# Performance work log

Measured on AMD Instinct MI355X. Metric: run time of the kernel, lower is better.

## Reference

```python
import jax, jax.numpy as jnp
import numpy as np

EPS = 0.05        # idw eps from __init__
RMS_EPS = 1e-6    # rmsnorm eps
B, NTOT, N, GS, C = 128, 129, 128, 16, 384


def setup_inputs() -> dict:
    key = jax.random.key(0)
    k1, k2, k3, k4 = jax.random.split(key, 4)
    f = jax.random.normal(k1, (B, NTOT, C), dtype=jnp.float32)
    distance = jax.random.uniform(k2, (B, N, GS), dtype=jnp.float32)
    rf = jax.random.normal(k3, (NTOT, C), dtype=jnp.float32)
    knorm_w = jnp.ones((C,), dtype=jnp.float32)
    idx = jax.random.randint(k4, (B, N, GS), 0, B * N, dtype=jnp.int64)
    return {"f": f, "distance": distance, "rf": rf, "knorm_w": knorm_w, "idx": idx}


def _rmsnorm(x, w):
    rms = jnp.sqrt(jnp.mean(x * x, axis=-1, keepdims=True) + RMS_EPS)
    return x / rms * w


def reference(f, distance, rf, knorm_w, idx):
    t = f.shape[1] - N                       # number of cls tokens (1)
    cls_token = f[:, :t, :]                  # [B, t, C]
    x = f[:, t:, :]                          # [B, 128, C]
    rfx = rf[t:]                             # [128, C]
    c = rfx                                  # adabias: per-point bias broadcast over batch
    bsz, n_pts, ch = x.shape
    # gather neighbors: flat index into [B*128, C]
    nf = x.reshape(-1, ch)[idx.reshape(-1)].reshape(bsz, n_pts, GS, ch)
    nf = nf - x[:, :, None, :]               # centering
    fb = c + x                               # bias-shifted center features
    # inverse-distance weights over group dim
    w = 1.0 / (distance + EPS)
    w = w / jnp.sum(w, axis=-1, keepdims=True)
    sf = jnp.sum(w[..., None] * nf, axis=2)  # [B, 128, C]
    out = fb + _rmsnorm(sf, knorm_w)
    return jnp.concatenate([cls_token, out], axis=1)
```

## Files before the change

### kernel.cpp

```cpp
#include <hip/hip_runtime.h>

#define EPSW 0.05f
#define RMS_EPS 1e-6f
#define NB 128
#define NTOT 129
#define NN 128
#define GS 16
#define NC 384
#define NROWS (NB * NN)

#define XQ_OFF 65536

static __device__ __forceinline__ float i8f(unsigned u, int sh) {
    return (float)(int)(char)(u >> sh);
}

__global__ __launch_bounds__(256) void pack_kernel(const float* __restrict__ f,
                                                   float* __restrict__ scales,
                                                   unsigned char* __restrict__ xq)
{
    const int row  = (blockIdx.x << 2) | (threadIdx.x >> 6);
    const int lane = threadIdx.x & 63;
    const int b = row >> 7, n = row & 127;
    const bool act = lane < 48;

    const float* src = f + ((size_t)b * NTOT + 1 + n) * NC;
    float v0=0,v1=0,v2=0,v3=0,v4=0,v5=0,v6=0,v7=0;
    float m = 0.0f;
    if (act) {
        const float4 p0 = *(const float4*)(src + lane * 8);
        const float4 p1 = *(const float4*)(src + lane * 8 + 4);
        v0=p0.x; v1=p0.y; v2=p0.z; v3=p0.w;
        v4=p1.x; v5=p1.y; v6=p1.z; v7=p1.w;
        m = fmaxf(fmaxf(fmaxf(fabsf(v0),fabsf(v1)),fmaxf(fabsf(v2),fabsf(v3))),
                  fmaxf(fmaxf(fabsf(v4),fabsf(v5)),fmaxf(fabsf(v6),fabsf(v7))));
    }
    #pragma unroll
    for (int o = 32; o > 0; o >>= 1) m = fmaxf(m, __shfl_xor(m, o));
    m = fmaxf(m, 1e-20f);
    const float inv = 127.0f / m;
    if (lane == 0) scales[row] = m * (1.0f / 127.0f);
    if (act) {
        unsigned lo = 0, hi = 0;
        lo |= ((unsigned)((int)rintf(v0*inv) & 0xff));
        lo |= ((unsigned)((int)rintf(v1*inv) & 0xff)) << 8;
        lo |= ((unsigned)((int)rintf(v2*inv) & 0xff)) << 16;
        lo |= ((unsigned)((int)rintf(v3*inv) & 0xff)) << 24;
        hi |= ((unsigned)((int)rintf(v4*inv) & 0xff));
        hi |= ((unsigned)((int)rintf(v5*inv) & 0xff)) << 8;
        hi |= ((unsigned)((int)rintf(v6*inv) & 0xff)) << 16;
        hi |= ((unsigned)((int)rintf(v7*inv) & 0xff)) << 24;
        uint2 u; u.x = lo; u.y = hi;
        *(uint2*)(xq + (size_t)row * 384 + lane * 8) = u;
    }
}

__global__ __launch_bounds__(256) void rectify_kernel(
    const float* __restrict__ f,
    const float* __restrict__ distance,
    const float* __restrict__ rf,
    const float* __restrict__ knorm,
    const int* __restrict__ idx,
    const float* __restrict__ scales,
    const unsigned char* __restrict__ xq,
    float* __restrict__ out)
{
    const int wave = threadIdx.x >> 6;
    const int lane = threadIdx.x & 63;
    const int bn   = (blockIdx.x << 2) | wave;
    const int b    = bn >> 7;
    const int n    = bn & 127;
    const bool act = lane < 48;
    const int lact = (lane < 47) ? lane : 47;
    const int c0   = lane * 8;

    const int g16 = lane & 15;
    const float w = 1.0f / (distance[(size_t)bn * GS + g16] + EPSW);
    float s = w;
    s += __shfl_xor(s, 1); s += __shfl_xor(s, 2);
    s += __shfl_xor(s, 4); s += __shfl_xor(s, 8);
    const int   ri  = idx[(size_t)bn * GS + g16];
    const float wns = (w / s) * scales[ri];

    float4 x0 = make_float4(0,0,0,0), x1 = make_float4(0,0,0,0);
    const float* xrow = f + ((size_t)b * NTOT + 1 + n) * NC + c0;
    if (act) {
        x0 = *(const float4*)(xrow);
        x1 = *(const float4*)(xrow + 4);
        if (n == 0) {
            const float* cs = f + (size_t)b * NTOT * NC + c0;
            float*       cd = out + (size_t)b * NTOT * NC + c0;
            *(float4*)(cd)     = *(const float4*)(cs);
            *(float4*)(cd + 4) = *(const float4*)(cs + 4);
        }
    }

    float a0=0,a1=0,a2=0,a3=0,a4=0,a5=0,a6=0,a7=0;
    #pragma unroll
    for (int g = 0; g < GS; ++g) {
        const int   r  = __shfl(ri, g);
        const float ws = __shfl(wns, g);
        const uint2 u  = *(const uint2*)(xq + (size_t)r * 384 + lact * 8);
        a0 += ws * i8f(u.x, 0);
        a1 += ws * i8f(u.x, 8);
        a2 += ws * i8f(u.x, 16);
        a3 += ws * i8f(u.x, 24);
        a4 += ws * i8f(u.y, 0);
        a5 += ws * i8f(u.y, 8);
        a6 += ws * i8f(u.y, 16);
        a7 += ws * i8f(u.y, 24);
    }
    a0 -= x0.x; a1 -= x0.y; a2 -= x0.z; a3 -= x0.w;
    a4 -= x1.x; a5 -= x1.y; a6 -= x1.z; a7 -= x1.w;

    float ss = act ? (a0*a0 + a1*a1 + a2*a2 + a3*a3 +
                      a4*a4 + a5*a5 + a6*a6 + a7*a7) : 0.0f;
    #pragma unroll
    for (int o = 32; o > 0; o >>= 1) ss += __shfl_xor(ss, o);
    const float rinv = rsqrtf(ss * (1.0f / (float)NC) + RMS_EPS);

    if (act) {
        const float* rfrow = rf + (size_t)(1 + n) * NC + c0;
        const float4 r0 = *(const float4*)(rfrow);
        const float4 r1 = *(const float4*)(rfrow + 4);
        const float4 k0 = *(const float4*)(knorm + c0);
        const float4 k1 = *(const float4*)(knorm + c0 + 4);

        float4 o0, o1;
        o0.x = r0.x + x0.x + a0 * rinv * k0.x;
        o0.y = r0.y + x0.y + a1 * rinv * k0.y;
        o0.z = r0.z + x0.z + a2 * rinv * k0.z;
        o0.w = r0.w + x0.w + a3 * rinv * k0.w;
        o1.x = r1.x + x1.x + a4 * rinv * k1.x;
        o1.y = r1.y + x1.y + a5 * rinv * k1.y;
        o1.z = r1.z + x1.z + a6 * rinv * k1.z;
        o1.w = r1.w + x1.w + a7 * rinv * k1.w;

        float* orow = out + ((size_t)b * NTOT + 1 + n) * NC + c0;
        *(float4*)(orow)     = o0;
        *(float4*)(orow + 4) = o1;
    }
}

extern "C" void kernel_launch(void* const* d_in, const int* in_sizes, int n_in,
                              void* d_out, int out_size, void* d_ws, size_t ws_size,
                              hipStream_t stream) {
    const float* f        = (const float*)d_in[0];
    const float* distance = (const float*)d_in[1];
    const float* rf       = (const float*)d_in[2];
    const float* knorm    = (const float*)d_in[3];
    const int*   idx      = (const int*)d_in[4];
    float*       out      = (float*)d_out;

    float*         scales = (float*)d_ws;
    unsigned char* xq     = (unsigned char*)d_ws + XQ_OFF;

    pack_kernel<<<NROWS / 4, 256, 0, stream>>>(f, scales, xq);
    rectify_kernel<<<NROWS / 4, 256, 0, stream>>>(
        f, distance, rf, knorm, idx, scales, xq, out);
}
```

Before: 101.0 us.

## Fuse pack and rectify into one cooperative kernel with grid sync

Merges the int8 pack pass and the gather/RMSNorm pass into a single cooperative kernel that uses a grid-wide barrier between the phases. Each wave handles four rows and keeps its fp32 center rows in registers, so f is not read a second time and one kernel launch is removed. Falls back to the two-kernel path if the cooperative launch fails. This adds the cost of a grid sync and higher register pressure, and the grid of 1024 blocks must be fully co-resident.

Result: slower. 397.4 us (+293.5%).

```diff
diff --git a/kernel.cpp b/kernel.cpp
--- a/kernel.cpp
+++ b/kernel.cpp
@@ -1,4 +1,5 @@
 #include <hip/hip_runtime.h>
+#include <hip/hip_cooperative_groups.h>
 
 #define EPSW 0.05f
 #define RMS_EPS 1e-6f
@@ -15,6 +16,141 @@
     return (float)(int)(char)(u >> sh);
 }
 
+__global__ __launch_bounds__(256, 4) void fused_kernel(
+    const float* __restrict__ f,
+    const float* __restrict__ distance,
+    const float* __restrict__ rf,
+    const float* __restrict__ knorm,
+    const int* __restrict__ idx,
+    float* __restrict__ scales,
+    unsigned char* __restrict__ xq,
+    float* __restrict__ out)
+{
+    const int wave = threadIdx.x >> 6;
+    const int lane = threadIdx.x & 63;
+    const int row0 = (blockIdx.x << 4) | (wave << 2);
+    const bool act = lane < 48;
+    const int lact = (lane < 47) ? lane : 47;
+    const int c0   = lane * 8;
+    const int g16  = lane & 15;
+
+    float xr[4][8];
+    float wn[4];
+    int   ri[4];
+
+    #pragma unroll
+    for (int r = 0; r < 4; ++r) {
+        const int row = row0 + r;
+        const int b = row >> 7, n = row & 127;
+
+        const float w = 1.0f / (distance[(size_t)row * GS + g16] + EPSW);
+        float s = w;
+        s += __shfl_xor(s, 1); s += __shfl_xor(s, 2);
+        s += __shfl_xor(s, 4); s += __shfl_xor(s, 8);
+        wn[r] = w / s;
+        ri[r] = idx[(size_t)row * GS + g16];
+
+        const float* src = f + ((size_t)b * NTOT + 1 + n) * NC;
+        float m = 0.0f;
+        if (act) {
+            const float4 p0 = *(const float4*)(src + c0);
+            const float4 p1 = *(const float4*)(src + c0 + 4);
+            xr[r][0]=p0.x; xr[r][1]=p0.y; xr[r][2]=p0.z; xr[r][3]=p0.w;
+            xr[r][4]=p1.x; xr[r][5]=p1.y; xr[r][6]=p1.z; xr[r][7]=p1.w;
+            #pragma unroll
+            for (int j = 0; j < 8; ++j) m = fmaxf(m, fabsf(xr[r][j]));
+        } else {
+            #pragma unroll
+            for (int j = 0; j < 8; ++j) xr[r][j] = 0.0f;
+        }
+        #pragma unroll
+        for (int o = 32; o > 0; o >>= 1) m = fmaxf(m, __shfl_xor(m, o));
+        m = fmaxf(m, 1e-20f);
+        const float inv = 127.0f / m;
+        if (lane == 0) scales[row] = m * (1.0f / 127.0f);
+        if (act) {
+            unsigned lo = 0, hi = 0;
+            lo |= ((unsigned)((int)rintf(xr[r][0]*inv) & 0xff));
+            lo |= ((unsigned)((int)rintf(xr[r][1]*inv) & 0xff)) << 8;
+            lo |= ((unsigned)((int)rintf(xr[r][2]*inv) & 0xff)) << 16;
+            lo |= ((unsigned)((int)rintf(xr[r][3]*inv) & 0xff)) << 24;
+            hi |= ((unsigned)((int)rintf(xr[r][4]*inv) & 0xff));
+            hi |= ((unsigned)((int)rintf(xr[r][5]*inv) & 0xff)) << 8;
+            hi |= ((unsigned)((int)rintf(xr[r][6]*inv) & 0xff)) << 16;
+            hi |= ((unsigned)((int)rintf(xr[r][7]*inv) & 0xff)) << 24;
+            uint2 u; u.x = lo; u.y = hi;
+            *(uint2*)(xq + (size_t)row * 384 + lane * 8) = u;
+        }
+
+        if (n == 0 && act) {
+            const float* cs = f + (size_t)b * NTOT * NC + c0;
+            float*       cd = out + (size_t)b * NTOT * NC + c0;
+            *(float4*)(cd)     = *(const float4*)(cs);
+            *(float4*)(cd + 4) = *(const float4*)(cs + 4);
+        }
+    }
+
+    __threadfence();
+    cooperative_groups::this_grid().sync();
+    __threadfence();
+
+    float4 k0 = make_float4(0,0,0,0), k1 = make_float4(0,0,0,0);
+    if (act) {
+        k0 = *(const float4*)(knorm + c0);
+        k1 = *(const float4*)(knorm + c0 + 4);
+    }
+
+    #pragma unroll
+    for (int r = 0; r < 4; ++r) {
+        const int row = row0 + r;
+        const int b = row >> 7, n = row & 127;
+
+        const float wns = wn[r] * scales[ri[r]];
+
+        float a0=0,a1=0,a2=0,a3=0,a4=0,a5=0,a6=0,a7=0;
+        #pragma unroll
+        for (int g = 0; g < GS; ++g) {
+            const int   rr = __shfl(ri[r], g);
+            const float ws = __shfl(wns, g);
+            const uint2 u  = *(const uint2*)(xq + (size_t)rr * 384 + lact * 8);
+            a0 += ws * i8f(u.x, 0);
+            a1 += ws * i8f(u.x, 8);
+            a2 += ws * i8f(u.x, 16);
+            a3 += ws * i8f(u.x, 24);
+            a4 += ws * i8f(u.y, 0);
+            a5 += ws * i8f(u.y, 8);
+            a6 += ws * i8f(u.y, 16);
+            a7 += ws * i8f(u.y, 24);
+        }
+        a0 -= xr[r][0]; a1 -= xr[r][1]; a2 -= xr[r][2]; a3 -= xr[r][3];
+        a4 -= xr[r][4]; a5 -= xr[r][5]; a6 -= xr[r][6]; a7 -= xr[r][7];
+
+        float ss = act ? (a0*a0 + a1*a1 + a2*a2 + a3*a3 +
+                          a4*a4 + a5*a5 + a6*a6 + a7*a7) : 0.0f;
+        #pragma unroll
+        for (int o = 32; o > 0; o >>= 1) ss += __shfl_xor(ss, o);
+        const float rinv = rsqrtf(ss * (1.0f / (float)NC) + RMS_EPS);
+
+        if (act) {
+            const float* rfrow = rf + (size_t)(1 + n) * NC + c0;
+            const float4 r0 = *(const float4*)(rfrow);
+            const float4 r1 = *(const float4*)(rfrow + 4);
+            float4 o0, o1;
+            o0.x = r0.x + xr[r][0] + a0 * rinv * k0.x;
+            o0.y = r0.y + xr[r][1] + a1 * rinv * k0.y;
+            o0.z = r0.z + xr[r][2] + a2 * rinv * k0.z;
+            o0.w = r0.w + xr[r][3] + a3 * rinv * k0.w;
+            o1.x = r1.x + xr[r][4] + a4 * rinv * k1.x;
+            o1.y = r1.y + xr[r][5] + a5 * rinv * k1.y;
+            o1.z = r1.z + xr[r][6] + a6 * rinv * k1.z;
+            o1.w = r1.w + xr[r][7] + a7 * rinv * k1.w;
+            float* orow = out + ((size_t)b * NTOT + 1 + n) * NC + c0;
+            *(float4*)(orow)     = o0;
+            *(float4*)(orow + 4) = o1;
+        }
+    }
+}
+
 __global__ __launch_bounds__(256) void pack_kernel(const float* __restrict__ f,
                                                    float* __restrict__ scales,
                                                    unsigned char* __restrict__ xq)
@@ -25,15 +161,17 @@
     const bool act = lane < 48;
 
     const float* src = f + ((size_t)b * NTOT + 1 + n) * NC;
-    float v0=0,v1=0,v2=0,v3=0,v4=0,v5=0,v6=0,v7=0;
-    float m = 0.0f;
+    float v[8]; float m = 0.0f;
     if (act) {
         const float4 p0 = *(const float4*)(src + lane * 8);
         const float4 p1 = *(const float4*)(src + lane * 8 + 4);
-        v0=p0.x; v1=p0.y; v2=p0.z; v3=p0.w;
-        v4=p1.x; v5=p1.y; v6=p1.z; v7=p1.w;
-        m = fmaxf(fmaxf(fmaxf(fabsf(v0),fabsf(v1)),fmaxf(fabsf(v2),fabsf(v3))),
-                  fmaxf(fmaxf(fabsf(v4),fabsf(v5)),fmaxf(fabsf(v6),fabsf(v7))));
+        v[0]=p0.x; v[1]=p0.y; v[2]=p0.z; v[3]=p0.w;
+        v[4]=p1.x; v[5]=p1.y; v[6]=p1.z; v[7]=p1.w;
+        #pragma unroll
+        for (int j = 0; j < 8; ++j) m = fmaxf(m, fabsf(v[j]));
+    } else {
+        #pragma unroll
+        for (int j = 0; j < 8; ++j) v[j] = 0.0f;
     }
     #pragma unroll
     for (int o = 32; o > 0; o >>= 1) m = fmaxf(m, __shfl_xor(m, o));
@@ -42,14 +180,14 @@
     if (lane == 0) scales[row] = m * (1.0f / 127.0f);
     if (act) {
         unsigned lo = 0, hi = 0;
-        lo |= ((unsigned)((int)rintf(v0*inv) & 0xff));
-        lo |= ((unsigned)((int)rintf(v1*inv) & 0xff)) << 8;
-        lo |= ((unsigned)((int)rintf(v2*inv) & 0xff)) << 16;
-        lo |= ((unsigned)((int)rintf(v3*inv) & 0xff)) << 24;
-        hi |= ((unsigned)((int)rintf(v4*inv) & 0xff));
-        hi |= ((unsigned)((int)rintf(v5*inv) & 0xff)) << 8;
-        hi |= ((unsigned)((int)rintf(v6*inv) & 0xff)) << 16;
-        hi |= ((unsigned)((int)rintf(v7*inv) & 0xff)) << 24;
+        lo |= ((unsigned)((int)rintf(v[0]*inv) & 0xff));
+        lo |= ((unsigned)((int)rintf(v[1]*inv) & 0xff)) << 8;
+        lo |= ((unsigned)((int)rintf(v[2]*inv) & 0xff)) << 16;
+        lo |= ((unsigned)((int)rintf(v[3]*inv) & 0xff)) << 24;
+        hi |= ((unsigned)((int)rintf(v[4]*inv) & 0xff));
+        hi |= ((unsigned)((int)rintf(v[5]*inv) & 0xff)) << 8;
+        hi |= ((unsigned)((int)rintf(v[6]*inv) & 0xff)) << 16;
+        hi |= ((unsigned)((int)rintf(v[7]*inv) & 0xff)) << 24;
         uint2 u; u.x = lo; u.y = hi;
         *(uint2*)(xq + (size_t)row * 384 + lane * 8) = u;
     }
@@ -125,7 +263,6 @@
         const float4 r1 = *(const float4*)(rfrow + 4);
         const float4 k0 = *(const float4*)(knorm + c0);
         const float4 k1 = *(const float4*)(knorm + c0 + 4);
-
         float4 o0, o1;
         o0.x = r0.x + x0.x + a0 * rinv * k0.x;
         o0.y = r0.y + x0.y + a1 * rinv * k0.y;
@@ -135,7 +272,6 @@
         o1.y = r1.y + x1.y + a5 * rinv * k1.y;
         o1.z = r1.z + x1.z + a6 * rinv * k1.z;
         o1.w = r1.w + x1.w + a7 * rinv * k1.w;
-
         float* orow = out + ((size_t)b * NTOT + 1 + n) * NC + c0;
         *(float4*)(orow)     = o0;
         *(float4*)(orow + 4) = o1;
@@ -155,7 +291,14 @@
     float*         scales = (float*)d_ws;
     unsigned char* xq     = (unsigned char*)d_ws + XQ_OFF;
 
-    pack_kernel<<<NROWS / 4, 256, 0, stream>>>(f, scales, xq);
-    rectify_kernel<<<NROWS / 4, 256, 0, stream>>>(
-        f, distance, rf, knorm, idx, scales, xq, out);
-}
+    void* args[] = { (void*)&f, (void*)&distance, (void*)&rf, (void*)&knorm,
+                     (void*)&idx, (void*)&scales, (void*)&xq, (void*)&out };
+    hipError_t e = hipLaunchCooperativeKernel((void*)fused_kernel,
+                                              dim3(NROWS / 16), dim3(256),
+                                              args, 0, stream);
+    if (e != hipSuccess) {
+        pack_kernel<<<NROWS / 4, 256, 0, stream>>>(f, scales, xq);
+        rectify_kernel<<<NROWS / 4, 256, 0, stream>>>(
+            f, distance, rf, knorm, idx, scales, xq, out);
+    }
+}
```
